# Performance work log

Hardware: AMD Instinct MI355X
Metric: run time of the kernel (lower is better)

## Reference

```python
import jax, jax.numpy as jnp
import numpy as np

S = 4096  # source_sequence_size
Q = 4096  # query_sequence_size
E = 2048  # embedding_size
D = 2048  # output_embedding_size


def setup_inputs() -> dict:
    key = jax.random.key(0)
    ks = jax.random.split(key, 9)
    s = 1.0 / np.sqrt(E)
    return {
        "key": jax.random.normal(ks[0], (S, E), jnp.float32),
        "value": jax.random.normal(ks[1], (S, E), jnp.float32),
        "query": jax.random.normal(ks[2], (Q, E), jnp.float32),
        "Wk": jax.random.normal(ks[3], (D, E), jnp.float32) * s,
        "bk": jax.random.normal(ks[4], (D,), jnp.float32) * 0.01,
        "Wq": jax.random.normal(ks[5], (D, E), jnp.float32) * s,
        "bq": jax.random.normal(ks[6], (D,), jnp.float32) * 0.01,
        "Wv": jax.random.normal(ks[7], (D, E), jnp.float32) * s,
        "bv": jax.random.normal(ks[8], (D,), jnp.float32) * 0.01,
    }


def reference(key, value, query, Wk, bk, Wq, bq, Wv, bv):
    # Linear projections (nn.Linear: x @ W.T + b)
    k = key @ Wk.T + bk      # [S, D]
    v = value @ Wv.T + bv    # [S, D]
    q = query @ Wq.T + bq    # [Q, D]
    # Per-query-token attention scores over all source tokens (schema BOTH),
    # then weighted sum over value rows -- vectorized form of the per-token
    # apply_attention_scores loop.
    scale = 1.0 / jnp.sqrt(jnp.asarray(D, q.dtype))
    scores = jax.nn.softmax(jnp.einsum("qd,sd->qs", q, k) * scale, axis=-1)  # [Q, S]
    return jnp.einsum("qs,sd->qd", scores, v)  # [Q, D]
```

## Files before the change

kernel.cpp:

```cpp
#include <hip/hip_runtime.h>

#define S_SEQ 4096
#define Q_SEQ 4096
#define E_DIM 2048
#define D_DIM 2048

typedef __bf16 bf16;
typedef __bf16 bf16x4 __attribute__((ext_vector_type(4)));
typedef __bf16 bf16x8 __attribute__((ext_vector_type(8)));
typedef float f32x4 __attribute__((ext_vector_type(4)));

__global__ __launch_bounds__(256) void cast6(
    const float* __restrict__ i0, const float* __restrict__ i1,
    const float* __restrict__ i2, const float* __restrict__ i3,
    const float* __restrict__ i4, const float* __restrict__ i5,
    bf16* __restrict__ o0, bf16* __restrict__ o1, bf16* __restrict__ o2,
    bf16* __restrict__ o3, bf16* __restrict__ o4, bf16* __restrict__ o5) {
  const float* in;
  bf16* out;
  int n4;
  switch (blockIdx.y) {
    case 0: in = i0; out = o0; n4 = (S_SEQ * E_DIM) / 4; break;
    case 1: in = i1; out = o1; n4 = (S_SEQ * E_DIM) / 4; break;
    case 2: in = i2; out = o2; n4 = (S_SEQ * E_DIM) / 4; break;
    case 3: in = i3; out = o3; n4 = (D_DIM * E_DIM) / 4; break;
    case 4: in = i4; out = o4; n4 = (D_DIM * E_DIM) / 4; break;
    default: in = i5; out = o5; n4 = (D_DIM * E_DIM) / 4; break;
  }
  int i = blockIdx.x * 256 + threadIdx.x;
  if (i < n4) {
    float4 v = reinterpret_cast<const float4*>(in)[i];
    bf16x4 o;
    o[0] = (bf16)v.x; o[1] = (bf16)v.y; o[2] = (bf16)v.z; o[3] = (bf16)v.w;
    *reinterpret_cast<bf16x4*>(out + 4 * (size_t)i) = o;
  }
}

__device__ __forceinline__ void async_copy16(const bf16* g, bf16* l) {
  __builtin_amdgcn_global_load_lds(
      (const __attribute__((address_space(1))) void*)g,
      (__attribute__((address_space(3))) void*)l, 16, 0, 0);
}

__device__ __forceinline__ void xcd_remap(int id, int nt, int& m, int& n) {
  int xcd = id & 7;
  int lid = id >> 3;
  m = (xcd & 3) * 4 + (lid & 3);
  n = (xcd >> 2) * (nt >> 1) + (lid >> 2);
}

__device__ __forceinline__ void stage_half(const bf16* __restrict__ G, int ld,
                                           int grow0, int k0, bf16* lds,
                                           int wave, int lane) {
#pragma unroll
  for (int s = 0; s < 2; ++s) {
    int c = (wave * 2 + s) * 64 + lane;
    int row = c >> 3;
    int kc = (c & 7) ^ (row & 7);
    const bf16* g = G + (size_t)(grow0 + row) * ld + k0 + kc * 8;
    async_copy16(g, lds + (size_t)(wave * 2 + s) * 512);
  }
}

#define BARRIER __builtin_amdgcn_s_barrier()
#define LGKM0 asm volatile("s_waitcnt lgkmcnt(0)" ::: "memory")
#define VMCNT4 asm volatile("s_waitcnt vmcnt(4)" ::: "memory")
#define VMCNT0 asm volatile("s_waitcnt vmcnt(0)" ::: "memory")

#define RD_A(buf, IP)                                                         \
  _Pragma("unroll") for (int ii = 0; ii < 2; ++ii)                            \
  _Pragma("unroll") for (int kk = 0; kk < 2; ++kk)                            \
      aR[ii][kk] = *(const bf16x8*)(&Als[buf][(size_t)(wRow + ((IP)*2 + ii) * 16 + lrow) * 64 + slotk[kk] * 8]);

#define RD_B(buf, JP, dst)                                                    \
  _Pragma("unroll") for (int jj = 0; jj < 2; ++jj)                            \
  _Pragma("unroll") for (int kk = 0; kk < 2; ++kk)                            \
      dst[jj][kk] = *(const bf16x8*)(&Bls[buf][(size_t)(wCol + ((JP)*2 + jj) * 16 + lrow) * 64 + slotk[kk] * 8]);

#define MMA(IP, JP, bsrc)                                                     \
  __builtin_amdgcn_s_setprio(1);                                              \
  _Pragma("unroll") for (int ii = 0; ii < 2; ++ii)                            \
  _Pragma("unroll") for (int jj = 0; jj < 2; ++jj)                            \
  _Pragma("unroll") for (int kk = 0; kk < 2; ++kk)                            \
      acc[(IP)*2 + ii][(JP)*2 + jj] = __builtin_amdgcn_mfma_f32_16x16x32_bf16( \
          aR[ii][kk], bsrc[jj][kk], acc[(IP)*2 + ii][(JP)*2 + jj], 0, 0, 0);  \
  __builtin_amdgcn_s_setprio(0)

template <int EPI>
__device__ __forceinline__ void gemm_body(
    const bf16* __restrict__ A, int lda,
    const bf16* __restrict__ B, int ldb,
    void* __restrict__ C, int ldc,
    const float* __restrict__ aux, float scale, int K, int mBase, int nBase) {
  __shared__ __align__(16) bf16 Als[2][256 * 64];
  __shared__ __align__(16) bf16 Bls[2][128 * 64];

  const int tid  = threadIdx.x;
  const int wave = tid >> 6;
  const int lane = tid & 63;
  const int quad = lane >> 4;
  const int lrow = lane & 15;
  const int wRow = (wave >> 1) * 64;
  const int wCol = (wave & 1) * 64;
  const int slotk[2] = {quad ^ (lrow & 7), (4 + quad) ^ (lrow & 7)};

  f32x4 acc[4][4];
#pragma unroll
  for (int i = 0; i < 4; ++i)
#pragma unroll
    for (int j = 0; j < 4; ++j) {
      f32x4 z = {0.f, 0.f, 0.f, 0.f};
      acc[i][j] = z;
    }

  bf16x8 aR[2][2], b0[2][2], b1[2][2];

  stage_half(B, ldb, nBase, 0, &Bls[0][0], wave, lane);
  stage_half(A, lda, mBase, 0, &Als[0][0], wave, lane);
  stage_half(A, lda, mBase + 128, 0, &Als[0][128 * 64], wave, lane);
  stage_half(B, ldb, nBase, 64, &Bls[1][0], wave, lane);
  stage_half(A, lda, mBase, 64, &Als[1][0], wave, lane);
  VMCNT4;
  BARRIER;

  const int NI = K >> 7;
#pragma unroll 1
  for (int i = 0; i < NI; ++i) {
    const bool nl = (i + 1 < NI);
    const int kb = i * 128;
    RD_A(0, 0);
    RD_B(0, 0, b0);
    stage_half(A, lda, mBase + 128, kb + 64, &Als[1][128 * 64], wave, lane);
    BARRIER; LGKM0; MMA(0, 0, b0); BARRIER;
    RD_B(0, 1, b1);
    BARRIER; LGKM0; MMA(0, 1, b1); BARRIER;
    RD_A(0, 1);
    if (nl) stage_half(B, ldb, nBase, kb + 128, &Bls[0][0], wave, lane);
    BARRIER; LGKM0; MMA(1, 1, b1); BARRIER;
    if (nl) {
      stage_half(A, lda, mBase, kb + 128, &Als[0][0], wave, lane);
      VMCNT4;
    } else {
      VMCNT0;
    }
    BARRIER; LGKM0; MMA(1, 0, b0); BARRIER;
    RD_A(1, 0);
    RD_B(1, 0, b0);
    if (nl) stage_half(A, lda, mBase + 128, kb + 128, &Als[0][128 * 64], wave, lane);
    BARRIER; LGKM0; MMA(0, 0, b0); BARRIER;
    RD_B(1, 1, b1);
    BARRIER; LGKM0; MMA(0, 1, b1); BARRIER;
    RD_A(1, 1);
    if (nl) stage_half(B, ldb, nBase, kb + 192, &Bls[1][0], wave, lane);
    BARRIER; LGKM0; MMA(1, 1, b1); BARRIER;
    if (nl) {
      stage_half(A, lda, mBase, kb + 192, &Als[1][0], wave, lane);
      VMCNT4;
    }
    BARRIER; LGKM0; MMA(1, 0, b0); BARRIER;
  }

  float rinv[4][4];
  if (EPI == 2) {
#pragma unroll
    for (int i = 0; i < 4; ++i)
#pragma unroll
      for (int r = 0; r < 4; ++r)
        rinv[i][r] = aux[mBase + wRow + i * 16 + quad * 4 + r];
  }
#pragma unroll
  for (int j = 0; j < 4; ++j) {
    const int cn = nBase + wCol + j * 16 + lrow;
    float bj = 0.f;
    if (EPI == 0) bj = aux[cn];
#pragma unroll
    for (int i = 0; i < 4; ++i) {
      const int rbase = mBase + wRow + i * 16 + quad * 4;
#pragma unroll
      for (int r = 0; r < 4; ++r) {
        if (EPI == 0)
          ((bf16*)C)[(size_t)(rbase + r) * ldc + cn] = (bf16)(acc[i][j][r] + bj);
        else if (EPI == 1)
          ((bf16*)C)[(size_t)(rbase + r) * ldc + cn] =
              (bf16)__expf(acc[i][j][r] * scale);
        else
          ((float*)C)[(size_t)(rbase + r) * ldc + cn] = acc[i][j][r] * rinv[i][r];
      }
    }
  }
}

__global__ __launch_bounds__(512, 2) void qk_gemm(
    const bf16* __restrict__ A, const bf16* __restrict__ B,
    bf16* __restrict__ E, float scale) {
  int m, n;
  xcd_remap(blockIdx.x, 32, m, n);
  gemm_body<1>(A, D_DIM, B, D_DIM, (void*)E, S_SEQ, nullptr, scale, D_DIM,
               m * 256, n * 128);
}

__global__ __launch_bounds__(512, 2) void pv_gemm(
    const bf16* __restrict__ E, const bf16* __restrict__ vT,
    float* __restrict__ out, const float* __restrict__ inv) {
  int m, n;
  xcd_remap(blockIdx.x, 16, m, n);
  gemm_body<2>(E, S_SEQ, vT, S_SEQ, (void*)out, D_DIM, inv, 0.f, S_SEQ,
               m * 256, n * 128);
}

__global__ __launch_bounds__(512, 2) void proj_gemm(
    const bf16* __restrict__ xk, const bf16* __restrict__ xq,
    const bf16* __restrict__ xv,
    const bf16* __restrict__ Wk, const bf16* __restrict__ Wq,
    const bf16* __restrict__ Wv,
    const float* __restrict__ bk, const float* __restrict__ bq,
    const float* __restrict__ bv,
    bf16* __restrict__ ok, bf16* __restrict__ oq, bf16* __restrict__ ov) {
  const bf16 *A, *W;
  const float* b;
  bf16* o;
  switch (blockIdx.z) {
    case 0: A = xk; W = Wk; b = bk; o = ok; break;
    case 1: A = xq; W = Wq; b = bq; o = oq; break;
    default: A = xv; W = Wv; b = bv; o = ov; break;
  }
  int m, n;
  xcd_remap(blockIdx.x, 16, m, n);
  gemm_body<0>(A, E_DIM, W, E_DIM, (void*)o, D_DIM, b, 0.f, E_DIM,
               m * 256, n * 128);
}

__global__ __launch_bounds__(256) void transpose_bf16(
    const bf16* __restrict__ in, bf16* __restrict__ out) {
  __shared__ bf16 tile[64][66];
  const int t = threadIdx.x;
  const int c0 = blockIdx.x * 64;
  const int r0 = blockIdx.y * 64;
  const int col = t & 63;
  const int r4 = t >> 6;
#pragma unroll
  for (int i = 0; i < 16; ++i) {
    int rr = i * 4 + r4;
    tile[rr][col] = in[(size_t)(r0 + rr) * D_DIM + c0 + col];
  }
  __syncthreads();
#pragma unroll
  for (int i = 0; i < 16; ++i) {
    int rr = i * 4 + r4;
    out[(size_t)(c0 + rr) * S_SEQ + r0 + col] = tile[col][rr];
  }
}

__global__ __launch_bounds__(256) void rowsum_inv(
    const bf16* __restrict__ E, float* __restrict__ inv) {
  const int t = threadIdx.x;
  const int wave = t >> 6;
  const int lane = t & 63;
  const int row = blockIdx.x * 4 + wave;
  const bf16x8* src = (const bf16x8*)(E + (size_t)row * S_SEQ);
  float s = 0.f;
#pragma unroll
  for (int i = 0; i < 8; ++i) {
    bf16x8 v = src[lane + i * 64];
#pragma unroll
    for (int j = 0; j < 8; ++j) s += (float)v[j];
  }
#pragma unroll
  for (int off = 32; off > 0; off >>= 1)
    s += __shfl_down(s, off, 64);
  if (lane == 0) inv[row] = 1.0f / s;
}

extern "C" void kernel_launch(void* const* d_in, const int* in_sizes, int n_in,
                              void* d_out, int out_size, void* d_ws, size_t ws_size,
                              hipStream_t stream) {
  const float* key   = (const float*)d_in[0];
  const float* value = (const float*)d_in[1];
  const float* query = (const float*)d_in[2];
  const float* Wk = (const float*)d_in[3];
  const float* bk = (const float*)d_in[4];
  const float* Wq = (const float*)d_in[5];
  const float* bq = (const float*)d_in[6];
  const float* Wv = (const float*)d_in[7];
  const float* bv = (const float*)d_in[8];

  const size_t MB = 1ull << 20;
  char* ws = (char*)d_ws;
  bf16* key_bf   = (bf16*)(ws + 0 * MB);
  bf16* value_bf = (bf16*)(ws + 16 * MB);
  bf16* query_bf = (bf16*)(ws + 32 * MB);
  bf16* Wk_bf    = (bf16*)(ws + 48 * MB);
  bf16* Wq_bf    = (bf16*)(ws + 56 * MB);
  bf16* Wv_bf    = (bf16*)(ws + 64 * MB);
  bf16* k_bf     = (bf16*)(ws + 72 * MB);
  bf16* q_bf     = (bf16*)(ws + 88 * MB);
  bf16* v_bf     = (bf16*)(ws + 104 * MB);
  bf16* vT_bf    = (bf16*)(ws + 120 * MB);
  bf16* E        = (bf16*)(ws + 0 * MB);
  float* inv     = (float*)(ws + 34 * MB);

  dim3 blk(256);
  dim3 blk512(512);

  cast6<<<dim3(8192, 6), blk, 0, stream>>>(
      key, value, query, Wk, Wq, Wv,
      key_bf, value_bf, query_bf, Wk_bf, Wq_bf, Wv_bf);

  proj_gemm<<<dim3(256, 1, 3), blk512, 0, stream>>>(
      key_bf, query_bf, value_bf, Wk_bf, Wq_bf, Wv_bf, bk, bq, bv,
      k_bf, q_bf, v_bf);

  transpose_bf16<<<dim3(D_DIM / 64, S_SEQ / 64), blk, 0, stream>>>(v_bf, vT_bf);

  const float scale = 0.022097086912079608f;
  qk_gemm<<<dim3(512), blk512, 0, stream>>>(q_bf, k_bf, E, scale);

  rowsum_inv<<<dim3(1024), blk, 0, stream>>>(E, inv);

  pv_gemm<<<dim3(256), blk512, 0, stream>>>(E, vT_bf, (float*)d_out, inv);
}
```

Before: 471.8 us.

## Restructure GEMM main loop into four 16-MFMA phases with fewer barriers

Reorganizes the ping-pong GEMM inner loop from eight 8-MFMA phases into four 16-MFMA phases. Both B fragments are loaded together, which halves the barrier/lgkmcnt wait count per K-step. The schedule of async global-to-LDS staging and the vmcnt wait depth (4 to 2) are changed so that both A halves are issued together. This lowers synchronization overhead per MFMA. In exchange, loads are prefetched less far ahead, which could expose memory latency, and register pressure rises.

```diff
diff --git a/kernel.cpp b/kernel.cpp
--- a/kernel.cpp
+++ b/kernel.cpp
@@ -64,7 +64,7 @@
 
 #define BARRIER __builtin_amdgcn_s_barrier()
 #define LGKM0 asm volatile("s_waitcnt lgkmcnt(0)" ::: "memory")
-#define VMCNT4 asm volatile("s_waitcnt vmcnt(4)" ::: "memory")
+#define VMCNT2 asm volatile("s_waitcnt vmcnt(2)" ::: "memory")
 #define VMCNT0 asm volatile("s_waitcnt vmcnt(0)" ::: "memory")
 
 #define RD_A(buf, IP)                                                         \
@@ -77,13 +77,18 @@
   _Pragma("unroll") for (int kk = 0; kk < 2; ++kk)                            \
       dst[jj][kk] = *(const bf16x8*)(&Bls[buf][(size_t)(wCol + ((JP)*2 + jj) * 16 + lrow) * 64 + slotk[kk] * 8]);
 
-#define MMA(IP, JP, bsrc)                                                     \
-  __builtin_amdgcn_s_setprio(1);                                              \
-  _Pragma("unroll") for (int ii = 0; ii < 2; ++ii)                            \
-  _Pragma("unroll") for (int jj = 0; jj < 2; ++jj)                            \
-  _Pragma("unroll") for (int kk = 0; kk < 2; ++kk)                            \
-      acc[(IP)*2 + ii][(JP)*2 + jj] = __builtin_amdgcn_mfma_f32_16x16x32_bf16( \
-          aR[ii][kk], bsrc[jj][kk], acc[(IP)*2 + ii][(JP)*2 + jj], 0, 0, 0);  \
+#define MMA16(IP)                                                              \
+  __builtin_amdgcn_s_setprio(1);                                               \
+  _Pragma("unroll") for (int jj = 0; jj < 2; ++jj)                             \
+  _Pragma("unroll") for (int ii = 0; ii < 2; ++ii)                             \
+  _Pragma("unroll") for (int kk = 0; kk < 2; ++kk)                             \
+      acc[(IP)*2 + ii][jj] = __builtin_amdgcn_mfma_f32_16x16x32_bf16(          \
+          aR[ii][kk], b0[jj][kk], acc[(IP)*2 + ii][jj], 0, 0, 0);              \
+  _Pragma("unroll") for (int jj = 0; jj < 2; ++jj)                             \
+  _Pragma("unroll") for (int ii = 0; ii < 2; ++ii)                             \
+  _Pragma("unroll") for (int kk = 0; kk < 2; ++kk)                             \
+      acc[(IP)*2 + ii][2 + jj] = __builtin_amdgcn_mfma_f32_16x16x32_bf16(      \
+          aR[ii][kk], b1[jj][kk], acc[(IP)*2 + ii][2 + jj], 0, 0, 0);          \
   __builtin_amdgcn_s_setprio(0)
 
 template <int EPI>
@@ -119,8 +124,7 @@
   stage_half(A, lda, mBase, 0, &Als[0][0], wave, lane);
   stage_half(A, lda, mBase + 128, 0, &Als[0][128 * 64], wave, lane);
   stage_half(B, ldb, nBase, 64, &Bls[1][0], wave, lane);
-  stage_half(A, lda, mBase, 64, &Als[1][0], wave, lane);
-  VMCNT4;
+  VMCNT2;
   BARRIER;
 
   const int NI = K >> 7;
@@ -130,34 +134,32 @@
     const int kb = i * 128;
     RD_A(0, 0);
     RD_B(0, 0, b0);
+    RD_B(0, 1, b1);
+    stage_half(A, lda, mBase, kb + 64, &Als[1][0], wave, lane);
     stage_half(A, lda, mBase + 128, kb + 64, &Als[1][128 * 64], wave, lane);
-    BARRIER; LGKM0; MMA(0, 0, b0); BARRIER;
-    RD_B(0, 1, b1);
-    BARRIER; LGKM0; MMA(0, 1, b1); BARRIER;
+    BARRIER; LGKM0; MMA16(0); BARRIER;
     RD_A(0, 1);
-    if (nl) stage_half(B, ldb, nBase, kb + 128, &Bls[0][0], wave, lane);
-    BARRIER; LGKM0; MMA(1, 1, b1); BARRIER;
+    if (nl) {
+      stage_half(B, ldb, nBase, kb + 128, &Bls[0][0], wave, lane);
+      VMCNT2;
+    } else {
+      VMCNT0;
+    }
+    BARRIER; LGKM0; MMA16(1); BARRIER;
+    RD_A(1, 0);
+    RD_B(1, 0, b0);
+    RD_B(1, 1, b1);
     if (nl) {
       stage_half(A, lda, mBase, kb + 128, &Als[0][0], wave, lane);
-      VMCNT4;
-    } else {
-      VMCNT0;
-    }
-    BARRIER; LGKM0; MMA(1, 0, b0); BARRIER;
-    RD_A(1, 0);
-    RD_B(1, 0, b0);
-    if (nl) stage_half(A, lda, mBase + 128, kb + 128, &Als[0][128 * 64], wave, lane);
-    BARRIER; LGKM0; MMA(0, 0, b0); BARRIER;
-    RD_B(1, 1, b1);
-    BARRIER; LGKM0; MMA(0, 1, b1); BARRIER;
+      stage_half(A, lda, mBase + 128, kb + 128, &Als[0][128 * 64], wave, lane);
+    }
+    BARRIER; LGKM0; MMA16(0); BARRIER;
     RD_A(1, 1);
-    if (nl) stage_half(B, ldb, nBase, kb + 192, &Bls[1][0], wave, lane);
-    BARRIER; LGKM0; MMA(1, 1, b1); BARRIER;
     if (nl) {
-      stage_half(A, lda, mBase, kb + 192, &Als[1][0], wave, lane);
-      VMCNT4;
-    }
-    BARRIER; LGKM0; MMA(1, 0, b0); BARRIER;
+      stage_half(B, ldb, nBase, kb + 192, &Bls[1][0], wave, lane);
+      VMCNT2;
+    }
+    BARRIER; LGKM0; MMA16(1); BARRIER;
   }
 
   float rinv[4][4];
```

New measurement: 423.7 us. 10.2% less time.
